# Performance work log

Hardware: AMD Instinct MI355X
Metric: run time of the kernel (lower is better)

## Reference

```python
import jax, jax.numpy as jnp
import numpy as np

D_MODEL = 1024
N_HEADS = 16
ADAPTIVE_TEMP = 1.0
LN_EPS = 1e-5


def _sinusoidal_pe(max_len, d_model):
    pos = np.arange(max_len)[:, None].astype(np.float32)
    div = np.exp(np.arange(0, d_model, 2).astype(np.float32) * (-np.log(10000.0) / d_model))
    pe = np.zeros((max_len, d_model), dtype=np.float32)
    pe[:, 0::2] = np.sin(pos * div)
    pe[:, 1::2] = np.cos(pos * div)
    return jnp.asarray(pe)


def _mlp2(q, w1, b1, w2, b2):
    # Linear(1,h) -> ReLU -> Linear(h,d)
    return jax.nn.relu(q @ w1 + b1) @ w2 + b2


def setup_inputs() -> dict:
    key = jax.random.key(0)
    ks = jax.random.split(key, 24)
    B, T, D = 2, 2048, D_MODEL
    H2 = D // 2
    s = 0.02
    inp = {
        "x": jax.random.normal(ks[0], (B, T, D), jnp.float32),
        "quantile": jax.random.uniform(ks[1], (B, 1), jnp.float32),
        "quantile_importance": jax.random.uniform(ks[2], (100,), jnp.float32),
        "Wq": jax.random.normal(ks[3], (D, D), jnp.float32) * s,
        "bq": jnp.zeros((D,), jnp.float32),
        "Wk": jax.random.normal(ks[4], (D, D), jnp.float32) * s,
        "bk": jnp.zeros((D,), jnp.float32),
        "Wv": jax.random.normal(ks[5], (D, D), jnp.float32) * s,
        "bv": jnp.zeros((D,), jnp.float32),
        "Wo": jax.random.normal(ks[6], (D, D), jnp.float32) * s,
        "bo": jnp.zeros((D,), jnp.float32),
        "qpq_w1": jax.random.normal(ks[7], (1, H2), jnp.float32) * s,
        "qpq_b1": jnp.zeros((H2,), jnp.float32),
        "qpq_w2": jax.random.normal(ks[8], (H2, D), jnp.float32) * s,
        "qpq_b2": jnp.zeros((D,), jnp.float32),
        "qpk_w1": jax.random.normal(ks[9], (1, H2), jnp.float32) * s,
        "qpk_b1": jnp.zeros((H2,), jnp.float32),
        "qpk_w2": jax.random.normal(ks[10], (H2, D), jnp.float32) * s,
        "qpk_b2": jnp.zeros((D,), jnp.float32),
        "qpv_w1": jax.random.normal(ks[11], (1, H2), jnp.float32) * s,
        "qpv_b1": jnp.zeros((H2,), jnp.float32),
        "qpv_w2": jax.random.normal(ks[12], (H2, D), jnp.float32) * s,
        "qpv_b2": jnp.zeros((D,), jnp.float32),
        "ln_g": jnp.ones((D,), jnp.float32),
        "ln_b": jnp.zeros((D,), jnp.float32),
    }
    return inp


def reference(x, quantile, quantile_importance,
              Wq, bq, Wk, bk, Wv, bv, Wo, bo,
              qpq_w1, qpq_b1, qpq_w2, qpq_b2,
              qpk_w1, qpk_b1, qpk_w2, qpk_b2,
              qpv_w1, qpv_b1, qpv_w2, qpv_b2,
              ln_g, ln_b):
    B, T, D = x.shape
    H = N_HEADS
    dk = D // H

    # positional encoding
    x = x + _sinusoidal_pe(T, D)

    # quantile-conditioned embeddings [B, D]
    q_embed = _mlp2(quantile, qpq_w1, qpq_b1, qpq_w2, qpq_b2)
    k_embed = _mlp2(quantile, qpk_w1, qpk_b1, qpk_w2, qpk_b2)
    v_embed = _mlp2(quantile, qpv_w1, qpv_b1, qpv_w2, qpv_b2)

    # importance weight per batch (no-grad buffer lookup)
    buf = jax.lax.stop_gradient(quantile_importance)
    idx = jnp.clip((quantile[:, 0] * 100).astype(jnp.int32), 0, 99)
    mx = buf.max()
    imp = buf[idx]
    imp = jnp.where(mx > 0, imp / mx, imp)  # [B]

    Q = (x @ Wq + bq) + q_embed[:, None, :]
    K = (x @ Wk + bk) + k_embed[:, None, :]
    V = (x @ Wv + bv) + v_embed[:, None, :]

    # [B, H, T, dk]
    Q = Q.reshape(B, T, H, dk).transpose(0, 2, 1, 3)
    K = K.reshape(B, T, H, dk).transpose(0, 2, 1, 3)
    V = V.reshape(B, T, H, dk).transpose(0, 2, 1, 3)

    scores = jnp.einsum('bhtd,bhsd->bhts', Q, K) / jnp.sqrt(jnp.float32(dk))
    scale = 1.0 + imp * ADAPTIVE_TEMP  # [B]
    scores = scores * scale[:, None, None, None]

    attn = jax.nn.softmax(scores, axis=-1)  # dropout is identity at inference
    out = jnp.einsum('bhts,bhsd->bhtd', attn, V)
    out = out.transpose(0, 2, 1, 3).reshape(B, T, D)
    out = out @ Wo + bo

    y = x + out
    mu = y.mean(axis=-1, keepdims=True)
    var = y.var(axis=-1, keepdims=True)
    return (y - mu) / jnp.sqrt(var + LN_EPS) * ln_g + ln_b
```

## Files before the change

kernel.cpp:

```cpp
#include <hip/hip_runtime.h>

#define D 1024
#define T 2048
#define BATCH 2
#define NR 4096
#define NH 16
#define HID 512

typedef unsigned short u16;
typedef unsigned int u32;
typedef unsigned long long u64;
typedef float f32x4 __attribute__((ext_vector_type(4)));
typedef __bf16 bf16x8 __attribute__((ext_vector_type(8)));

__device__ __forceinline__ u16 f2bf(float f) {
    union { __bf16 h; u16 u; } c; c.h = (__bf16)f; return c.u;
}

__device__ __forceinline__ u32 cvtpk(float a, float b) {
    u32 r;
    asm("v_cvt_pk_bf16_f32 %0, %1, %2" : "=v"(r) : "v"(a), "v"(b));
    return r;
}

__device__ __forceinline__ void gload16(const u16* g, u16* l) {
    __builtin_amdgcn_global_load_lds(
        (const __attribute__((address_space(1))) unsigned int*)g,
        (__attribute__((address_space(3))) unsigned int*)l,
        16, 0, 0);
}

__global__ __launch_bounds__(256) void k_mlp1(const float* __restrict__ qtl,
        const float* __restrict__ w1q, const float* __restrict__ b1q, const float* __restrict__ w2q,
        const float* __restrict__ w1k, const float* __restrict__ b1k, const float* __restrict__ w2k,
        const float* __restrict__ w1v, const float* __restrict__ b1v, const float* __restrict__ w2v,
        const float* __restrict__ qimp, float* __restrict__ part, float* __restrict__ scl)
{
    int dc = blockIdx.x;
    int jc = blockIdx.y;
    int wb = blockIdx.z;
    int which = wb >> 1, b = wb & 1;
    const float *w1, *b1, *w2;
    if (which == 0)      { w1 = w1q; b1 = b1q; w2 = w2q; }
    else if (which == 1) { w1 = w1k; b1 = b1k; w2 = w2k; }
    else                 { w1 = w1v; b1 = b1v; w2 = w2v; }
    int tid = threadIdx.x;
    __shared__ float h[128];
    if (tid < 128) {
        int j = jc * 128 + tid;
        h[tid] = fmaxf(qtl[b] * w1[j] + b1[j], 0.0f);
    }
    __syncthreads();
    int d = dc * 256 + tid;
    float acc = 0.0f;
    for (int j = 0; j < 128; ++j) acc += h[j] * w2[(size_t)(jc * 128 + j) * D + d];
    part[((size_t)wb * 4 + jc) * D + d] = acc;
    if (dc == 0 && jc == 0 && wb == 0 && tid < BATCH) {
        float mx = qimp[0];
        for (int i = 1; i < 100; ++i) mx = fmaxf(mx, qimp[i]);
        float q = qtl[tid];
        int idx = (int)(q * 100.0f);
        idx = idx < 0 ? 0 : (idx > 99 ? 99 : idx);
        float imp = qimp[idx];
        if (mx > 0.0f) imp /= mx;
        scl[tid] = 1.0f + imp;
    }
}

__global__ __launch_bounds__(256) void k_mlp2(const float* __restrict__ part,
        const float* __restrict__ b2q, const float* __restrict__ b2k, const float* __restrict__ b2v,
        float* __restrict__ embeds)
{
    int dc = blockIdx.x;
    int wb = blockIdx.y;
    int which = wb >> 1;
    const float* b2 = which == 0 ? b2q : which == 1 ? b2k : b2v;
    int d = dc * 256 + threadIdx.x;
    float acc = b2[d];
    #pragma unroll
    for (int jc = 0; jc < 4; ++jc) acc += part[((size_t)wb * 4 + jc) * D + d];
    embeds[(size_t)wb * D + d] = acc;
}

__global__ __launch_bounds__(256) void k_pe(const float* __restrict__ x,
                                            float* __restrict__ xpe, u16* __restrict__ xpeb)
{
    int idx = (blockIdx.x * 256 + threadIdx.x) * 4;
    int d = idx & (D - 1);
    int t = (idx >> 10) & (T - 1);
    const float KL = -0.0089944731946f;
    float ft = (float)t;
    float dv0 = __expf((float)d * KL);
    float dv1 = __expf((float)(d + 2) * KL);
    float a0 = ft * dv0, a1 = ft * dv1;
    float4 xv = *reinterpret_cast<const float4*>(x + idx);
    float4 r;
    r.x = xv.x + __sinf(a0);
    r.y = xv.y + __cosf(a0);
    r.z = xv.z + __sinf(a1);
    r.w = xv.w + __cosf(a1);
    *reinterpret_cast<float4*>(xpe + idx) = r;
    ushort4 o;
    o.x = f2bf(r.x); o.y = f2bf(r.y); o.z = f2bf(r.z); o.w = f2bf(r.w);
    *reinterpret_cast<ushort4*>(xpeb + idx) = o;
}

__global__ __launch_bounds__(256) void k_wconv(const float* __restrict__ Wq, const float* __restrict__ Wk,
                                               const float* __restrict__ Wv, const float* __restrict__ Wo,
                                               u16* __restrict__ Wt)
{
    __shared__ float tile[64][65];
    int z = blockIdx.z;
    const float* W = z == 0 ? Wq : z == 1 ? Wk : z == 2 ? Wv : Wo;
    u16* out = Wt + (size_t)z * D * D;
    int n0 = blockIdx.x * 64, k0 = blockIdx.y * 64;
    int r = threadIdx.x >> 4;
    int c4 = (threadIdx.x & 15) * 4;
    #pragma unroll
    for (int rr = 0; rr < 64; rr += 16) {
        float4 v = *reinterpret_cast<const float4*>(W + (size_t)(k0 + r + rr) * D + n0 + c4);
        tile[r + rr][c4 + 0] = v.x; tile[r + rr][c4 + 1] = v.y;
        tile[r + rr][c4 + 2] = v.z; tile[r + rr][c4 + 3] = v.w;
    }
    __syncthreads();
    #pragma unroll
    for (int rr = 0; rr < 64; rr += 16) {
        ushort4 o;
        o.x = f2bf(tile[c4 + 0][r + rr]);
        o.y = f2bf(tile[c4 + 1][r + rr]);
        o.z = f2bf(tile[c4 + 2][r + rr]);
        o.w = f2bf(tile[c4 + 3][r + rr]);
        *reinterpret_cast<ushort4*>(out + (size_t)(n0 + r + rr) * D + k0 + c4) = o;
    }
}

__device__ __forceinline__ void gemm128(const u16* __restrict__ Ag, const u16* __restrict__ Bg,
                                        int m0, int n0, f32x4 acc[4][4])
{
    __shared__ u16 As[128 * 64];
    __shared__ u16 Bs[128 * 64];
    const int tid = threadIdx.x;
    const int lane = tid & 63, wave = tid >> 6;
    const int wr = wave >> 1, wc = wave & 1;
    #pragma unroll
    for (int i = 0; i < 4; ++i)
        #pragma unroll
        for (int j = 0; j < 4; ++j)
            #pragma unroll
            for (int e = 0; e < 4; ++e) acc[i][j][e] = 0.0f;

    for (int kt = 0; kt < 16; ++kt) {
        __syncthreads();
        #pragma unroll
        for (int c = 0; c < 4; ++c) {
            int ci = c * 256 + tid;
            int row = ci >> 3;
            int sl = (ci & 7) ^ (row & 7);
            gload16(Ag + (size_t)(m0 + row) * D + kt * 64 + sl * 8, As + (size_t)ci * 8);
            gload16(Bg + (size_t)(n0 + row) * D + kt * 64 + sl * 8, Bs + (size_t)ci * 8);
        }
        __syncthreads();
        #pragma unroll
        for (int ks = 0; ks < 2; ++ks) {
            bf16x8 af[4], bfr[4];
            #pragma unroll
            for (int i = 0; i < 4; ++i) {
                int ra = wr * 64 + i * 16 + (lane & 15);
                int sa = ((ks * 4 + (lane >> 4)) ^ (ra & 7));
                af[i] = *reinterpret_cast<const bf16x8*>((const char*)As + ra * 128 + sa * 16);
                int rb = wc * 64 + i * 16 + (lane & 15);
                int sb = ((ks * 4 + (lane >> 4)) ^ (rb & 7));
                bfr[i] = *reinterpret_cast<const bf16x8*>((const char*)Bs + rb * 128 + sb * 16);
            }
            #pragma unroll
            for (int i = 0; i < 4; ++i)
                #pragma unroll
                for (int j = 0; j < 4; ++j)
                    acc[i][j] = __builtin_amdgcn_mfma_f32_16x16x32_bf16(af[i], bfr[j], acc[i][j], 0, 0, 0);
        }
    }
}

__global__ __launch_bounds__(256, 2)
void k_qkv(const u16* __restrict__ A, const u16* __restrict__ Wt,
           const float* __restrict__ bq, const float* __restrict__ bk, const float* __restrict__ bv,
           const float* __restrict__ embeds, const float* __restrict__ scl,
           u16* __restrict__ Qo, u16* __restrict__ Ko, u16* __restrict__ Vt)
{
    int which = blockIdx.z;
    const u16* Bg = Wt + (size_t)which * D * D;
    const float* bias = which == 0 ? bq : which == 1 ? bk : bv;
    const float* emb = embeds + which * (BATCH * D);
    int m0 = blockIdx.x * 128, n0 = blockIdx.y * 128;
    f32x4 acc[4][4];
    gemm128(A, Bg, m0, n0, acc);
    int lane = threadIdx.x & 63, wave = threadIdx.x >> 6;
    int wr = wave >> 1, wc = wave & 1;
    int rowbase = m0 + wr * 64 + ((lane >> 4) << 2);
    int colbase = n0 + wc * 64 + (lane & 15);
    if (which < 2) {
        u16* Out = which == 0 ? Qo : Ko;
        float sc0 = 1.0f, sc1 = 1.0f;
        if (which == 0) {
            sc0 = scl[0] * 0.125f * 1.44269504f;
            sc1 = scl[1] * 0.125f * 1.44269504f;
        }
        #pragma unroll
        for (int j = 0; j < 4; ++j) {
            int c = colbase + j * 16;
            float add0 = bias[c] + emb[c];
            float add1 = bias[c] + emb[D + c];
            #pragma unroll
            for (int i = 0; i < 4; ++i) {
                int rb = rowbase + i * 16;
                #pragma unroll
                for (int jj = 0; jj < 4; ++jj) {
                    int r = rb + jj;
                    float v = (r >> 11) ? (acc[i][j][jj] + add1) * sc1
                                        : (acc[i][j][jj] + add0) * sc0;
                    Out[(size_t)r * D + c] = f2bf(v);
                }
            }
        }
    } else {
        #pragma unroll
        for (int j = 0; j < 4; ++j) {
            int c = colbase + j * 16;
            int hh = c >> 6, cc = c & 63;
            float add0 = bias[c] + emb[c];
            float add1 = bias[c] + emb[D + c];
            #pragma unroll
            for (int i = 0; i < 4; ++i) {
                int rb = rowbase + i * 16;
                int bb = rb >> 11;
                int t = rb & (T - 1);
                float add = bb ? add1 : add0;
                ushort4 o;
                o.x = f2bf(acc[i][j][0] + add);
                o.y = f2bf(acc[i][j][1] + add);
                o.z = f2bf(acc[i][j][2] + add);
                o.w = f2bf(acc[i][j][3] + add);
                *reinterpret_cast<ushort4*>(Vt + ((size_t)((bb * NH + hh) * 64 + cc)) * T + t) = o;
            }
        }
    }
}

__global__ __launch_bounds__(512, 4)
void k_attn(const u16* __restrict__ Q, const u16* __restrict__ K, const u16* __restrict__ Vt,
            u16* __restrict__ AO)
{
    __shared__ u16 Ks[2][128 * 64];
    __shared__ u16 Vs[2][64 * 128];
    int bh = blockIdx.x;
    int b = bh >> 4, hh = bh & 15;
    int q0 = blockIdx.y * 128;
    int tid = threadIdx.x;
    int lane = tid & 63, wave = tid >> 6, g = lane >> 4;

    bf16x8 qf[2];
    {
        size_t off = (size_t)(b * T + q0 + wave * 16 + (lane & 15)) * D + hh * 64 + (g << 3);
        qf[0] = *reinterpret_cast<const bf16x8*>(Q + off);
        qf[1] = *reinterpret_cast<const bf16x8*>(Q + off + 32);
    }

    f32x4 o[4];
    #pragma unroll
    for (int j = 0; j < 4; ++j)
        #pragma unroll
        for (int e = 0; e < 4; ++e) o[j][e] = 0.0f;
    float m_run = -1e30f, l_run = 0.0f;

    #pragma unroll
    for (int c = 0; c < 2; ++c) {
        int ci = c * 512 + tid;
        int row = ci >> 3;
        int sl = (ci & 7) ^ (row & 7);
        gload16(K + (size_t)(b * T + row) * D + hh * 64 + sl * 8, Ks[0] + (size_t)ci * 8);
        int rowv = ci >> 4;
        int slv = (ci & 15) ^ (rowv & 7);
        gload16(Vt + (size_t)(bh * 64 + rowv) * T + slv * 8, Vs[0] + (size_t)ci * 8);
    }
    __syncthreads();

    for (int kt = 0; kt < 16; ++kt) {
        int cur = kt & 1;
        if (kt < 15) {
            int t0 = (kt + 1) * 128;
            #pragma unroll
            for (int c = 0; c < 2; ++c) {
                int ci = c * 512 + tid;
                int row = ci >> 3;
                int sl = (ci & 7) ^ (row & 7);
                gload16(K + (size_t)(b * T + t0 + row) * D + hh * 64 + sl * 8, Ks[cur ^ 1] + (size_t)ci * 8);
                int rowv = ci >> 4;
                int slv = (ci & 15) ^ (rowv & 7);
                gload16(Vt + (size_t)(bh * 64 + rowv) * T + t0 + slv * 8, Vs[cur ^ 1] + (size_t)ci * 8);
            }
        }
        const char* Ksc = (const char*)Ks[cur];
        const char* Vsc = (const char*)Vs[cur];
        f32x4 s[8];
        #pragma unroll
        for (int ni = 0; ni < 8; ++ni)
            #pragma unroll
            for (int e = 0; e < 4; ++e) s[ni][e] = 0.0f;
        __builtin_amdgcn_s_setprio(1);
        #pragma unroll
        for (int ks = 0; ks < 2; ++ks)
            #pragma unroll
            for (int ni = 0; ni < 8; ++ni) {
                int rk = ni * 16 + (lane & 15);
                int sp = (ks * 4 + g) ^ (rk & 7);
                bf16x8 kf = *reinterpret_cast<const bf16x8*>(Ksc + rk * 128 + sp * 16);
                s[ni] = __builtin_amdgcn_mfma_f32_16x16x32_bf16(kf, qf[ks], s[ni], 0, 0, 0);
            }
        __builtin_amdgcn_s_setprio(0);
        float mt = s[0][0];
        #pragma unroll
        for (int ni = 0; ni < 8; ++ni)
            #pragma unroll
            for (int e = 0; e < 4; ++e) mt = fmaxf(mt, s[ni][e]);
        mt = fmaxf(mt, __shfl_xor(mt, 16, 64));
        mt = fmaxf(mt, __shfl_xor(mt, 32, 64));
        bool skip = __all((int)(mt <= m_run + 11.0f));
        float corr = 1.0f;
        if (!skip) {
            float mn = fmaxf(m_run, mt);
            corr = __builtin_exp2f(m_run - mn);
            m_run = mn;
        }
        float psum = 0.0f;
        #pragma unroll
        for (int ni = 0; ni < 8; ++ni)
            #pragma unroll
            for (int e = 0; e < 4; ++e) {
                float p = __builtin_exp2f(s[ni][e] - m_run);
                s[ni][e] = p;
                psum += p;
            }
        psum += __shfl_xor(psum, 16, 64);
        psum += __shfl_xor(psum, 32, 64);
        if (!skip) {
            l_run = l_run * corr + psum;
            float c4[4];
            #pragma unroll
            for (int jr = 0; jr < 4; ++jr)
                c4[jr] = __shfl(corr, (lane & 48) | (g << 2) | jr, 64);
            #pragma unroll
            for (int j = 0; j < 4; ++j)
                #pragma unroll
                for (int jr = 0; jr < 4; ++jr) o[j][jr] *= c4[jr];
        } else {
            l_run += psum;
        }
        __builtin_amdgcn_s_setprio(1);
        #pragma unroll
        for (int kb = 0; kb < 4; ++kb) {
            union { bf16x8 v; u32 w[4]; } pa;
            pa.w[0] = cvtpk(s[2 * kb][0], s[2 * kb][1]);
            pa.w[1] = cvtpk(s[2 * kb][2], s[2 * kb][3]);
            pa.w[2] = cvtpk(s[2 * kb + 1][0], s[2 * kb + 1][1]);
            pa.w[3] = cvtpk(s[2 * kb + 1][2], s[2 * kb + 1][3]);
            #pragma unroll
            for (int j = 0; j < 4; ++j) {
                int rv = j * 16 + (lane & 15);
                int xm = rv & 7;
                const char* vb = Vsc + rv * 256 + (g & 1) * 8;
                union { bf16x8 v; u64 d[2]; } vf;
                vf.d[0] = *reinterpret_cast<const u64*>(vb + (((4 * kb + (g >> 1)) ^ xm) << 4));
                vf.d[1] = *reinterpret_cast<const u64*>(vb + (((4 * kb + (g >> 1) + 2) ^ xm) << 4));
                o[j] = __builtin_amdgcn_mfma_f32_16x16x32_bf16(pa.v, vf.v, o[j], 0, 0, 0);
            }
        }
        __builtin_amdgcn_s_setprio(0);
        __syncthreads();
    }
    float linv = 1.0f / l_run;
    float l4[4];
    #pragma unroll
    for (int jr = 0; jr < 4; ++jr)
        l4[jr] = __shfl(linv, (lane & 48) | (g << 2) | jr, 64);
    #pragma unroll
    for (int j = 0; j < 4; ++j)
        #pragma unroll
        for (int jr = 0; jr < 4; ++jr) {
            size_t off = (size_t)(b * T + q0 + wave * 16 + (g << 2) + jr) * D + hh * 64 + j * 16 + (lane & 15);
            AO[off] = f2bf(o[j][jr] * l4[jr]);
        }
}

__global__ __launch_bounds__(256, 2)
void k_ogemm(const u16* __restrict__ A, const u16* __restrict__ Wt,
             const float* __restrict__ bo, const float* __restrict__ xpe,
             float* __restrict__ y)
{
    int m0 = blockIdx.x * 128, n0 = blockIdx.y * 128;
    f32x4 acc[4][4];
    gemm128(A, Wt, m0, n0, acc);
    int lane = threadIdx.x & 63, wave = threadIdx.x >> 6;
    int wr = wave >> 1, wc = wave & 1;
    int rowbase = m0 + wr * 64 + ((lane >> 4) << 2);
    int colbase = n0 + wc * 64 + (lane & 15);
    #pragma unroll
    for (int j = 0; j < 4; ++j) {
        int c = colbase + j * 16;
        float bc = bo[c];
        #pragma unroll
        for (int i = 0; i < 4; ++i) {
            #pragma unroll
            for (int jj = 0; jj < 4; ++jj) {
                int r = rowbase + i * 16 + jj;
                y[(size_t)r * D + c] = acc[i][j][jj] + bc + xpe[(size_t)r * D + c];
            }
        }
    }
}

__global__ __launch_bounds__(256) void k_ln(const float* __restrict__ y, const float* __restrict__ g,
                                            const float* __restrict__ bb, float* __restrict__ out)
{
    int row = blockIdx.x;
    int tid = threadIdx.x;
    const float* yr = y + (size_t)row * D;
    float4 v = *reinterpret_cast<const float4*>(yr + tid * 4);
    float s = v.x + v.y + v.z + v.w;
    float s2 = v.x * v.x + v.y * v.y + v.z * v.z + v.w * v.w;
    #pragma unroll
    for (int off = 1; off < 64; off <<= 1) {
        s += __shfl_xor(s, off, 64);
        s2 += __shfl_xor(s2, off, 64);
    }
    __shared__ float red[8];
    int wave = tid >> 6, lane = tid & 63;
    if (lane == 0) { red[wave] = s; red[4 + wave] = s2; }
    __syncthreads();
    s = red[0] + red[1] + red[2] + red[3];
    s2 = red[4] + red[5] + red[6] + red[7];
    float mu = s * (1.0f / 1024.0f);
    float var = s2 * (1.0f / 1024.0f) - mu * mu;
    float rstd = rsqrtf(var + 1e-5f);
    float4 gv = *reinterpret_cast<const float4*>(g + tid * 4);
    float4 bv = *reinterpret_cast<const float4*>(bb + tid * 4);
    float4 o;
    o.x = (v.x - mu) * rstd * gv.x + bv.x;
    o.y = (v.y - mu) * rstd * gv.y + bv.y;
    o.z = (v.z - mu) * rstd * gv.z + bv.z;
    o.w = (v.w - mu) * rstd * gv.w + bv.w;
    *reinterpret_cast<float4*>(out + (size_t)row * D + tid * 4) = o;
}

extern "C" void kernel_launch(void* const* d_in, const int* in_sizes, int n_in,
                              void* d_out, int out_size, void* d_ws, size_t ws_size,
                              hipStream_t stream)
{
    const float* x    = (const float*)d_in[0];
    const float* qtl  = (const float*)d_in[1];
    const float* qimp = (const float*)d_in[2];
    const float* Wq = (const float*)d_in[3];
    const float* bq = (const float*)d_in[4];
    const float* Wk = (const float*)d_in[5];
    const float* bk = (const float*)d_in[6];
    const float* Wv = (const float*)d_in[7];
    const float* bv = (const float*)d_in[8];
    const float* Wo = (const float*)d_in[9];
    const float* bo = (const float*)d_in[10];
    const float* qpq_w1 = (const float*)d_in[11];
    const float* qpq_b1 = (const float*)d_in[12];
    const float* qpq_w2 = (const float*)d_in[13];
    const float* qpq_b2 = (const float*)d_in[14];
    const float* qpk_w1 = (const float*)d_in[15];
    const float* qpk_b1 = (const float*)d_in[16];
    const float* qpk_w2 = (const float*)d_in[17];
    const float* qpk_b2 = (const float*)d_in[18];
    const float* qpv_w1 = (const float*)d_in[19];
    const float* qpv_b1 = (const float*)d_in[20];
    const float* qpv_w2 = (const float*)d_in[21];
    const float* qpv_b2 = (const float*)d_in[22];
    const float* ln_g = (const float*)d_in[23];
    const float* ln_b = (const float*)d_in[24];
    (void)in_sizes; (void)n_in; (void)out_size; (void)ws_size;

    char* w = (char*)d_ws;
    float* xpe   = (float*)(w);
    u16* xpeb    = (u16*)(w + (16u << 20));
    u16* Wt      = (u16*)(w + (24u << 20));
    u16* Qb      = (u16*)(w + (32u << 20));
    u16* Kb      = (u16*)(w + (40u << 20));
    u16* Vtb     = (u16*)(w + (48u << 20));
    u16* AOb     = (u16*)(w + (56u << 20));
    float* yb    = (float*)(w + (32u << 20));
    float* emb   = (float*)(w + (64u << 20));
    float* scl   = (float*)(w + (64u << 20) + 32768);
    float* part  = (float*)(w + (64u << 20) + 65536);

    k_mlp1<<<dim3(4, 4, 6), 256, 0, stream>>>(qtl,
        qpq_w1, qpq_b1, qpq_w2,
        qpk_w1, qpk_b1, qpk_w2,
        qpv_w1, qpv_b1, qpv_w2,
        qimp, part, scl);
    k_mlp2<<<dim3(4, 6), 256, 0, stream>>>(part, qpq_b2, qpk_b2, qpv_b2, emb);
    k_pe<<<4096, 256, 0, stream>>>(x, xpe, xpeb);
    k_wconv<<<dim3(16, 16, 4), 256, 0, stream>>>(Wq, Wk, Wv, Wo, Wt);
    k_qkv<<<dim3(32, 8, 3), 256, 0, stream>>>(xpeb, Wt, bq, bk, bv, emb, scl, Qb, Kb, Vtb);
    k_attn<<<dim3(32, 16), 512, 0, stream>>>(Qb, Kb, Vtb, AOb);
    k_ogemm<<<dim3(32, 8), 256, 0, stream>>>(AOb, Wt + (size_t)3 * D * D, bo, xpe, yb);
    k_ln<<<4096, 256, 0, stream>>>(yb, ln_g, ln_b, (float*)d_out);
}
```

Baseline: 168.9 us.

## Switch attention to 32x32x16 MFMA with 4 waves of 32 query rows

Measured after the change: 162.4 us. 3.8% less time.

```diff
diff --git a/kernel.cpp b/kernel.cpp
--- a/kernel.cpp
+++ b/kernel.cpp
@@ -11,6 +11,7 @@
 typedef unsigned int u32;
 typedef unsigned long long u64;
 typedef float f32x4 __attribute__((ext_vector_type(4)));
+typedef float f32x16 __attribute__((ext_vector_type(16)));
 typedef __bf16 bf16x8 __attribute__((ext_vector_type(8)));
 
 __device__ __forceinline__ u16 f2bf(float f) {
@@ -21,6 +22,10 @@
     u32 r;
     asm("v_cvt_pk_bf16_f32 %0, %1, %2" : "=v"(r) : "v"(a), "v"(b));
     return r;
+}
+
+__device__ __forceinline__ void plswap(u32& x, u32& y) {
+    asm volatile("v_permlane32_swap_b32 %0, %1" : "+v"(x), "+v"(y));
 }
 
 __device__ __forceinline__ void gload16(const u16* g, u16* l) {
@@ -246,7 +251,7 @@
     }
 }
 
-__global__ __launch_bounds__(512, 4)
+__global__ __launch_bounds__(256, 2)
 void k_attn(const u16* __restrict__ Q, const u16* __restrict__ K, const u16* __restrict__ Vt,
             u16* __restrict__ AO)
 {
@@ -256,31 +261,31 @@
     int b = bh >> 4, hh = bh & 15;
     int q0 = blockIdx.y * 128;
     int tid = threadIdx.x;
-    int lane = tid & 63, wave = tid >> 6, g = lane >> 4;
-
-    bf16x8 qf[2];
+    int lane = tid & 63, w = tid >> 6;
+    int q31 = lane & 31, h = lane >> 5;
+
+    bf16x8 qf[4];
     {
-        size_t off = (size_t)(b * T + q0 + wave * 16 + (lane & 15)) * D + hh * 64 + (g << 3);
-        qf[0] = *reinterpret_cast<const bf16x8*>(Q + off);
-        qf[1] = *reinterpret_cast<const bf16x8*>(Q + off + 32);
-    }
-
-    f32x4 o[4];
-    #pragma unroll
-    for (int j = 0; j < 4; ++j)
-        #pragma unroll
-        for (int e = 0; e < 4; ++e) o[j][e] = 0.0f;
+        const u16* qp = Q + (size_t)(b * T + q0 + w * 32 + q31) * D + hh * 64 + h * 8;
+        #pragma unroll
+        for (int ds = 0; ds < 4; ++ds)
+            qf[ds] = *reinterpret_cast<const bf16x8*>(qp + ds * 16);
+    }
+
+    f32x16 o0, o1;
+    #pragma unroll
+    for (int e = 0; e < 16; ++e) { o0[e] = 0.0f; o1[e] = 0.0f; }
     float m_run = -1e30f, l_run = 0.0f;
 
     #pragma unroll
-    for (int c = 0; c < 2; ++c) {
-        int ci = c * 512 + tid;
+    for (int c = 0; c < 4; ++c) {
+        int ci = c * 256 + tid;
         int row = ci >> 3;
         int sl = (ci & 7) ^ (row & 7);
         gload16(K + (size_t)(b * T + row) * D + hh * 64 + sl * 8, Ks[0] + (size_t)ci * 8);
-        int rowv = ci >> 4;
-        int slv = (ci & 15) ^ (rowv & 7);
-        gload16(Vt + (size_t)(bh * 64 + rowv) * T + slv * 8, Vs[0] + (size_t)ci * 8);
+        int rv = ci >> 4;
+        int sv = (ci & 15) ^ (rv & 7);
+        gload16(Vt + (size_t)(bh * 64 + rv) * T + sv * 8, Vs[0] + (size_t)ci * 8);
     }
     __syncthreads();
 
@@ -289,106 +294,110 @@
         if (kt < 15) {
             int t0 = (kt + 1) * 128;
             #pragma unroll
-            for (int c = 0; c < 2; ++c) {
-                int ci = c * 512 + tid;
+            for (int c = 0; c < 4; ++c) {
+                int ci = c * 256 + tid;
                 int row = ci >> 3;
                 int sl = (ci & 7) ^ (row & 7);
                 gload16(K + (size_t)(b * T + t0 + row) * D + hh * 64 + sl * 8, Ks[cur ^ 1] + (size_t)ci * 8);
-                int rowv = ci >> 4;
-                int slv = (ci & 15) ^ (rowv & 7);
-                gload16(Vt + (size_t)(bh * 64 + rowv) * T + t0 + slv * 8, Vs[cur ^ 1] + (size_t)ci * 8);
+                int rv = ci >> 4;
+                int sv = (ci & 15) ^ (rv & 7);
+                gload16(Vt + (size_t)(bh * 64 + rv) * T + t0 + sv * 8, Vs[cur ^ 1] + (size_t)ci * 8);
             }
         }
         const char* Ksc = (const char*)Ks[cur];
         const char* Vsc = (const char*)Vs[cur];
-        f32x4 s[8];
-        #pragma unroll
-        for (int ni = 0; ni < 8; ++ni)
-            #pragma unroll
-            for (int e = 0; e < 4; ++e) s[ni][e] = 0.0f;
+
+        f32x16 s[4];
+        #pragma unroll
+        for (int k2 = 0; k2 < 4; ++k2)
+            #pragma unroll
+            for (int e = 0; e < 16; ++e) s[k2][e] = 0.0f;
         __builtin_amdgcn_s_setprio(1);
         #pragma unroll
-        for (int ks = 0; ks < 2; ++ks)
-            #pragma unroll
-            for (int ni = 0; ni < 8; ++ni) {
-                int rk = ni * 16 + (lane & 15);
-                int sp = (ks * 4 + g) ^ (rk & 7);
+        for (int k2 = 0; k2 < 4; ++k2) {
+            int rk = k2 * 32 + q31;
+            int xm = rk & 7;
+            #pragma unroll
+            for (int ds = 0; ds < 4; ++ds) {
+                int sp = (2 * ds + h) ^ xm;
                 bf16x8 kf = *reinterpret_cast<const bf16x8*>(Ksc + rk * 128 + sp * 16);
-                s[ni] = __builtin_amdgcn_mfma_f32_16x16x32_bf16(kf, qf[ks], s[ni], 0, 0, 0);
-            }
+                s[k2] = __builtin_amdgcn_mfma_f32_32x32x16_bf16(kf, qf[ds], s[k2], 0, 0, 0);
+            }
+        }
         __builtin_amdgcn_s_setprio(0);
-        float mt = s[0][0];
-        #pragma unroll
-        for (int ni = 0; ni < 8; ++ni)
-            #pragma unroll
-            for (int e = 0; e < 4; ++e) mt = fmaxf(mt, s[ni][e]);
-        mt = fmaxf(mt, __shfl_xor(mt, 16, 64));
+
+        float mt = -1e30f;
+        #pragma unroll
+        for (int k2 = 0; k2 < 4; ++k2)
+            #pragma unroll
+            for (int e = 0; e < 16; ++e) mt = fmaxf(mt, s[k2][e]);
         mt = fmaxf(mt, __shfl_xor(mt, 32, 64));
         bool skip = __all((int)(mt <= m_run + 11.0f));
-        float corr = 1.0f;
         if (!skip) {
             float mn = fmaxf(m_run, mt);
-            corr = __builtin_exp2f(m_run - mn);
+            float corr = __builtin_exp2f(m_run - mn);
             m_run = mn;
-        }
-        float psum = 0.0f;
-        #pragma unroll
-        for (int ni = 0; ni < 8; ++ni)
-            #pragma unroll
-            for (int e = 0; e < 4; ++e) {
-                float p = __builtin_exp2f(s[ni][e] - m_run);
-                s[ni][e] = p;
-                psum += p;
-            }
-        psum += __shfl_xor(psum, 16, 64);
+            l_run *= corr;
+            #pragma unroll
+            for (int reg = 0; reg < 16; ++reg) {
+                int src = ((reg & 3) + 8 * (reg >> 2)) + ((lane & 32) >> 3);
+                float cr = __shfl(corr, src, 64);
+                o0[reg] *= cr;
+                o1[reg] *= cr;
+            }
+        }
+        float ps0 = 0.0f, ps1 = 0.0f;
+        #pragma unroll
+        for (int k2 = 0; k2 < 4; ++k2)
+            #pragma unroll
+            for (int e = 0; e < 16; ++e) {
+                float p = __builtin_exp2f(s[k2][e] - m_run);
+                s[k2][e] = p;
+                if (k2 & 1) ps1 += p; else ps0 += p;
+            }
+        float psum = ps0 + ps1;
         psum += __shfl_xor(psum, 32, 64);
-        if (!skip) {
-            l_run = l_run * corr + psum;
-            float c4[4];
-            #pragma unroll
-            for (int jr = 0; jr < 4; ++jr)
-                c4[jr] = __shfl(corr, (lane & 48) | (g << 2) | jr, 64);
-            #pragma unroll
-            for (int j = 0; j < 4; ++j)
-                #pragma unroll
-                for (int jr = 0; jr < 4; ++jr) o[j][jr] *= c4[jr];
-        } else {
-            l_run += psum;
-        }
+        l_run += psum;
+
         __builtin_amdgcn_s_setprio(1);
         #pragma unroll
-        for (int kb = 0; kb < 4; ++kb) {
-            union { bf16x8 v; u32 w[4]; } pa;
-            pa.w[0] = cvtpk(s[2 * kb][0], s[2 * kb][1]);
-            pa.w[1] = cvtpk(s[2 * kb][2], s[2 * kb][3]);
-            pa.w[2] = cvtpk(s[2 * kb + 1][0], s[2 * kb + 1][1]);
-            pa.w[3] = cvtpk(s[2 * kb + 1][2], s[2 * kb + 1][3]);
-            #pragma unroll
-            for (int j = 0; j < 4; ++j) {
-                int rv = j * 16 + (lane & 15);
-                int xm = rv & 7;
-                const char* vb = Vsc + rv * 256 + (g & 1) * 8;
-                union { bf16x8 v; u64 d[2]; } vf;
-                vf.d[0] = *reinterpret_cast<const u64*>(vb + (((4 * kb + (g >> 1)) ^ xm) << 4));
-                vf.d[1] = *reinterpret_cast<const u64*>(vb + (((4 * kb + (g >> 1) + 2) ^ xm) << 4));
-                o[j] = __builtin_amdgcn_mfma_f32_16x16x32_bf16(pa.v, vf.v, o[j], 0, 0, 0);
-            }
+        for (int k2 = 0; k2 < 4; ++k2) {
+            u32 w0 = cvtpk(s[k2][0], s[k2][1]),   w1 = cvtpk(s[k2][2], s[k2][3]);
+            u32 w2 = cvtpk(s[k2][4], s[k2][5]),   w3 = cvtpk(s[k2][6], s[k2][7]);
+            u32 w4 = cvtpk(s[k2][8], s[k2][9]),   w5 = cvtpk(s[k2][10], s[k2][11]);
+            u32 w6 = cvtpk(s[k2][12], s[k2][13]), w7 = cvtpk(s[k2][14], s[k2][15]);
+            plswap(w0, w2); plswap(w1, w3);
+            plswap(w4, w6); plswap(w5, w7);
+            union { bf16x8 v; u32 u[4]; } plo, phi;
+            plo.u[0] = w0; plo.u[1] = w1; plo.u[2] = w2; plo.u[3] = w3;
+            phi.u[0] = w4; phi.u[1] = w5; phi.u[2] = w6; phi.u[3] = w7;
+            int rv0 = q31, rv1 = 32 + q31;
+            int x0 = rv0 & 7, x1 = rv1 & 7;
+            int klo = 2 * k2, khi = 2 * k2 + 1;
+            bf16x8 vf;
+            vf = *reinterpret_cast<const bf16x8*>(Vsc + rv0 * 256 + (((2 * klo + h) ^ x0) << 4));
+            o0 = __builtin_amdgcn_mfma_f32_32x32x16_bf16(plo.v, vf, o0, 0, 0, 0);
+            vf = *reinterpret_cast<const bf16x8*>(Vsc + rv1 * 256 + (((2 * klo + h) ^ x1) << 4));
+            o1 = __builtin_amdgcn_mfma_f32_32x32x16_bf16(plo.v, vf, o1, 0, 0, 0);
+            vf = *reinterpret_cast<const bf16x8*>(Vsc + rv0 * 256 + (((2 * khi + h) ^ x0) << 4));
+            o0 = __builtin_amdgcn_mfma_f32_32x32x16_bf16(phi.v, vf, o0, 0, 0, 0);
+            vf = *reinterpret_cast<const bf16x8*>(Vsc + rv1 * 256 + (((2 * khi + h) ^ x1) << 4));
+            o1 = __builtin_amdgcn_mfma_f32_32x32x16_bf16(phi.v, vf, o1, 0, 0, 0);
         }
         __builtin_amdgcn_s_setprio(0);
         __syncthreads();
     }
+
     float linv = 1.0f / l_run;
-    float l4[4];
-    #pragma unroll
-    for (int jr = 0; jr < 4; ++jr)
-        l4[jr] = __shfl(linv, (lane & 48) | (g << 2) | jr, 64);
-    #pragma unroll
-    for (int j = 0; j < 4; ++j)
-        #pragma unroll
-        for (int jr = 0; jr < 4; ++jr) {
-            size_t off = (size_t)(b * T + q0 + wave * 16 + (g << 2) + jr) * D + hh * 64 + j * 16 + (lane & 15);
-            AO[off] = f2bf(o[j][jr] * l4[jr]);
-        }
+    #pragma unroll
+    for (int reg = 0; reg < 16; ++reg) {
+        int src = ((reg & 3) + 8 * (reg >> 2)) + ((lane & 32) >> 3);
+        float li = __shfl(linv, src, 64);
+        int qr = q0 + w * 32 + (reg & 3) + 8 * (reg >> 2) + 4 * h;
+        size_t off = (size_t)(b * T + qr) * D + hh * 64 + q31;
+        AO[off] = f2bf(o0[reg] * li);
+        AO[off + 32] = f2bf(o1[reg] * li);
+    }
 }
 
 __global__ __launch_bounds__(256, 2)
@@ -504,7 +513,7 @@
     k_pe<<<4096, 256, 0, stream>>>(x, xpe, xpeb);
     k_wconv<<<dim3(16, 16, 4), 256, 0, stream>>>(Wq, Wk, Wv, Wo, Wt);
     k_qkv<<<dim3(32, 8, 3), 256, 0, stream>>>(xpeb, Wt, bq, bk, bv, emb, scl, Qb, Kb, Vtb);
-    k_attn<<<dim3(32, 16), 512, 0, stream>>>(Qb, Kb, Vtb, AOb);
+    k_attn<<<dim3(32, 16), 256, 0, stream>>>(Qb, Kb, Vtb, AOb);
     k_ogemm<<<dim3(32, 8), 256, 0, stream>>>(AOb, Wt + (size_t)3 * D * D, bo, xpe, yb);
     k_ln<<<4096, 256, 0, stream>>>(yb, ln_g, ln_b, (float*)d_out);
 }
```
